# Performance work log

Hardware: AMD Instinct MI355X
Metric: run time of the kernel (lower is better)

The kernel has to match this reference:

```python
import jax, jax.numpy as jnp
import numpy as np

BETA = 0.25
EPS = 1e-12

def setup_inputs() -> dict:
    key = jax.random.key(0)
    k1, k2 = jax.random.split(key)
    f_BChw = jax.random.normal(k1, (32, 64, 32, 32), dtype=jnp.float32)
    emb_weight = jax.random.normal(k2, (8192, 64), dtype=jnp.float32)
    return {"f_BChw": f_BChw, "emb_weight": emb_weight}

def reference(f_BChw, emb_weight):
    f = f_BChw.astype(jnp.float32)
    B, C, h, w = f.shape
    V = emb_weight.shape[0]
    # flatten tokens: [B,C,h,w] -> [N,C]
    NxC = jnp.transpose(f, (0, 2, 3, 1)).reshape(-1, C)
    # cosine nearest-neighbor on detached, L2-normalized queries/codes
    q = jax.lax.stop_gradient(NxC)
    q = q / jnp.maximum(jnp.linalg.norm(q, axis=-1, keepdims=True), EPS)
    wn = emb_weight / jnp.maximum(jnp.linalg.norm(emb_weight, axis=-1, keepdims=True), EPS)
    sim = q @ wn.T                      # [N,V] -- dominant memory traffic
    idx_N = jnp.argmax(sim, axis=1)     # [N]
    # gather codes -> [B,C,h,w]
    fhat = emb_weight[idx_N].reshape(B, h, w, C).transpose(0, 3, 1, 2)
    sg = jax.lax.stop_gradient
    vq_loss = BETA * jnp.mean((sg(fhat) - f) ** 2) + jnp.mean((fhat - sg(f)) ** 2)
    # straight-through estimator
    fhat_out = f + sg(fhat - f)
    # usage statistics (bincount)
    counts = jnp.zeros((V,), jnp.float32).at[idx_N].add(1.0)
    prob = counts / counts.sum()
    vocab_usage = jnp.mean((prob > 0.01 / V).astype(jnp.float32)) * 100.0
    entropy_loss = jnp.float32(0.0)
    return fhat_out, vq_loss, entropy_loss, vocab_usage
```

## Files before the change

kernel.cpp:

```cpp
#include <hip/hip_runtime.h>

typedef _Float16 f16x8 __attribute__((ext_vector_type(8)));
typedef float f32x16 __attribute__((ext_vector_type(16)));

#define V_TOTAL 8192
#define C_DIM   64
#define N_TOK   32768
#define VSPLIT  4
#define VSEG    (V_TOTAL / VSPLIT)
#define CHUNKS  (VSEG / 32)
#define INV2048 4.8828125e-4f

typedef const __attribute__((address_space(1))) _Float16 glb_f16;
typedef __attribute__((address_space(3))) _Float16 lds_f16;


__device__ __forceinline__ unsigned long long packkey(float s, int idx) {
    unsigned u = __float_as_uint(s);
    unsigned k = u ^ ((unsigned)(((int)u) >> 31) | 0x80000000u);
    return ((unsigned long long)k << 32) | (unsigned)(8191 - idx);
}

__global__ __launch_bounds__(256)
void k_prep(const float* __restrict__ w, _Float16* __restrict__ cp,
            unsigned long long* __restrict__ keys, int* __restrict__ counts) {
    int v = blockIdx.x * 256 + threadIdx.x;
    counts[v] = 0;
#pragma unroll
    for (int i = 0; i < 4; ++i) keys[v * 4 + i] = 0ull;
    const float4* row = (const float4*)(w + v * C_DIM);
    float4 r[16];
    float s = 0.f;
#pragma unroll
    for (int i = 0; i < 16; ++i) {
        r[i] = row[i];
        s += r[i].x * r[i].x + r[i].y * r[i].y + r[i].z * r[i].z + r[i].w * r[i].w;
    }
    float inv = 1.0f / fmaxf(sqrtf(s), 1e-12f);
    const float* rs = (const float*)r;
    const int cv = v >> 5, c = v & 31;
#pragma unroll
    for (int q = 0; q < 8; ++q) {
        f16x8 hi, lo;
#pragma unroll
        for (int j = 0; j < 8; ++j) {
            float x = rs[q * 8 + j] * inv;
            _Float16 h = (_Float16)x;
            hi[j] = h;
            lo[j] = (_Float16)((x - (float)h) * 2048.0f);
        }
        *(f16x8*)(cp + cv * 4096 +        q * 256 + c * 8) = hi;
        *(f16x8*)(cp + cv * 4096 + 2048 + q * 256 + c * 8) = lo;
    }
}

__global__ __launch_bounds__(256, 4)
void k_argmax(const float* __restrict__ f, const _Float16* __restrict__ cp,
              unsigned long long* __restrict__ keys) {
    __shared__ __align__(16) _Float16 lds[2][4096];

    const int tid  = threadIdx.x;
    const int lane = tid & 63;
    const int wid  = tid >> 6;
    const int c31  = lane & 31;
    const int g    = lane >> 5;
    const int seg  = blockIdx.y;
    const int t0   = blockIdx.x * 128 + wid * 32;

    f16x8 bh[4], bl[4];
    {
        const int T = t0 + c31;
        const float* fb = f + (T >> 10) * 65536 + (T & 1023);
#pragma unroll
        for (int ks = 0; ks < 4; ++ks) {
#pragma unroll
            for (int j = 0; j < 8; ++j) {
                float v = fb[(ks * 16 + g * 8 + j) * 1024];
                _Float16 h = (_Float16)v;
                bh[ks][j] = h;
                bl[ks][j] = (_Float16)((v - (float)h) * 2048.0f);
            }
        }
    }

    const _Float16* seg_cp = cp + (size_t)seg * (CHUNKS * 4096);

    auto stage = [&](int cv, int buf) {
        const _Float16* src = seg_cp + cv * 4096 + wid * 1024 + lane * 8;
        _Float16* dst = &lds[buf][wid * 1024];
        __builtin_amdgcn_global_load_lds((glb_f16*)src,       (lds_f16*)dst,       16, 0, 0);
        __builtin_amdgcn_global_load_lds((glb_f16*)(src+512), (lds_f16*)(dst+512), 16, 0, 0);
    };

    f32x16 am = {0.f,0.f,0.f,0.f,0.f,0.f,0.f,0.f,0.f,0.f,0.f,0.f,0.f,0.f,0.f,0.f};
    f32x16 ac = am;

    float best = -3.4e38f;
    int   bidx = 0;

    stage(0, 0);
    __syncthreads();

    for (int cv = 0; cv < CHUNKS; ++cv) {
        if (cv + 1 < CHUNKS) stage(cv + 1, (cv + 1) & 1);

        const _Float16* base = &lds[cv & 1][g * 256 + c31 * 8];
#pragma unroll
        for (int ks = 0; ks < 4; ++ks) {
            f16x8 AH = *(const f16x8*)(base + ks * 512);
            f16x8 AL = *(const f16x8*)(base + 2048 + ks * 512);
            am = __builtin_amdgcn_mfma_f32_32x32x16_f16(AH, bh[ks], am, 0, 0, 0);
            ac = __builtin_amdgcn_mfma_f32_32x32x16_f16(AH, bl[ks], ac, 0, 0, 0);
            ac = __builtin_amdgcn_mfma_f32_32x32x16_f16(AL, bh[ks], ac, 0, 0, 0);
        }

        const int codebase = seg * VSEG + cv * 32;
#pragma unroll
        for (int r = 0; r < 16; ++r) {
            const int codeq = codebase + (r & 3) + 8 * (r >> 2);
            float s = fmaf(ac[r], INV2048, am[r]);
            bool u = s > best;
            best = u ? s : best;
            bidx = u ? codeq : bidx;
            am[r] = 0.f;
            ac[r] = 0.f;
        }
        __syncthreads();
    }

    bidx += 4 * g;
    {
        float ov = __shfl_xor(best, 32);
        int   oi = __shfl_xor(bidx, 32);
        if (ov > best || (ov == best && oi < bidx)) { best = ov; bidx = oi; }
    }
    if (lane < 32) {
        atomicMax(&keys[t0 + c31], packkey(best, bidx));
    }
}

__global__ __launch_bounds__(256)
void k_finalize(const float* __restrict__ f, const float* __restrict__ w,
                const unsigned long long* __restrict__ keys,
                int* __restrict__ counts, float* __restrict__ blocksq,
                float* __restrict__ out) {
    const int tid = threadIdx.x;
    const int t   = blockIdx.x * 256 + tid;

    const int bi = 8191 - (int)(unsigned)(keys[t] & 0xFFFFFFFFull);
    atomicAdd(&counts[bi], 1);

    float4 cr[16];
    const float4* crow = (const float4*)(w + bi * C_DIM);
#pragma unroll
    for (int i = 0; i < 16; ++i) cr[i] = crow[i];
    const float* crs = (const float*)cr;

    const int bb = t >> 10;
    const int hw = t & 1023;
    const float* fb = f + bb * 65536 + hw;
    float*       ob = out + bb * 65536 + hw;

    float s = 0.f;
#pragma unroll
    for (int c = 0; c < C_DIM; ++c) {
        float fv = fb[c * 1024];
        float fh = crs[c];
        float d  = fh - fv;
        s += d * d;
        ob[c * 1024] = fv + d;
    }

    __shared__ float red[256];
    red[tid] = s;
    __syncthreads();
    for (int st = 128; st > 0; st >>= 1) {
        if (tid < st) red[tid] += red[tid + st];
        __syncthreads();
    }
    if (tid == 0) blocksq[blockIdx.x] = red[0];
}

__global__ __launch_bounds__(256)
void k_stats(const int* __restrict__ counts, const float* __restrict__ blocksq,
             float* __restrict__ out) {
    __shared__ float redf[256];
    __shared__ int   redi[256];
    const int tid = threadIdx.x;
    int used = 0;
    for (int v = tid; v < V_TOTAL; v += 256) used += (counts[v] > 0) ? 1 : 0;
    redi[tid] = used;
    redf[tid] = (tid < 128) ? blocksq[tid] : 0.f;
    __syncthreads();
    for (int st = 128; st > 0; st >>= 1) {
        if (tid < st) { redi[tid] += redi[tid + st]; redf[tid] += redf[tid + st]; }
        __syncthreads();
    }
    if (tid == 0) {
        float mse = redf[0] / 2097152.0f;
        out[2097152] = 0.25f * mse + mse;
        out[2097153] = 0.0f;
        out[2097154] = 100.0f * (float)redi[0] / 8192.0f;
    }
}

extern "C" void kernel_launch(void* const* d_in, const int* in_sizes, int n_in,
                              void* d_out, int out_size, void* d_ws, size_t ws_size,
                              hipStream_t stream) {
    const float* f = (const float*)d_in[0];
    const float* w = (const float*)d_in[1];
    float* out = (float*)d_out;
    float* ws  = (float*)d_ws;

    _Float16*           cp      = (_Float16*)ws;
    unsigned long long* keys    = (unsigned long long*)(ws + 524288);
    int*                counts  = (int*)(ws + 589824);
    float*              blocksq = ws + 598016;

    hipLaunchKernelGGL(k_prep, dim3(32), dim3(256), 0, stream, w, cp, keys, counts);
    hipLaunchKernelGGL(k_argmax, dim3(N_TOK / 128, VSPLIT), dim3(256), 0, stream,
                       f, cp, keys);
    hipLaunchKernelGGL(k_finalize, dim3(128), dim3(256), 0, stream,
                       f, w, keys, counts, blocksq, out);
    hipLaunchKernelGGL(k_stats, dim3(1), dim3(256), 0, stream,
                       counts, blocksq, out);
}
```

Baseline: 123.4 us.

## Two-pass argmax: fp16 screening with top-2 margin, exact rescoring of ambiguous tokens

Replaces the single split-fp16 (hi+lo, three MFMAs per step) argmax with a cheap first pass. That pass uses only hi fp16 products, tracks the top two scores per token, and deepens LDS staging to four buffers with explicit vmcnt waits. A classify kernel merges the per-segment top-2 values and accepts a token when the margin exceeds a threshold scaled by the query norm. Otherwise it appends the token to a list that a second kernel rescans with the full hi/lo precision. This aims to cut the MFMA work by about a third for most tokens. The cost is two extra launches, extra workspace traffic, and correctness that depends on the error-bound threshold holding.

```diff
diff --git a/kernel.cpp b/kernel.cpp
--- a/kernel.cpp
+++ b/kernel.cpp
@@ -6,10 +6,15 @@
 #define V_TOTAL 8192
 #define C_DIM   64
 #define N_TOK   32768
-#define VSPLIT  4
-#define VSEG    (V_TOTAL / VSPLIT)
-#define CHUNKS  (VSEG / 32)
 #define INV2048 4.8828125e-4f
+#define THR_COEF 2.2e-3f
+
+#define VSPLIT1 4
+#define VSEG1   2048
+#define CH1     32
+#define VSPLIT2 8
+#define VSEG2   1024
+#define CH2     32
 
 typedef const __attribute__((address_space(1))) _Float16 glb_f16;
 typedef __attribute__((address_space(3))) _Float16 lds_f16;
@@ -23,9 +28,11 @@
 
 __global__ __launch_bounds__(256)
 void k_prep(const float* __restrict__ w, _Float16* __restrict__ cp,
-            unsigned long long* __restrict__ keys, int* __restrict__ counts) {
+            unsigned long long* __restrict__ keys, int* __restrict__ counts,
+            int* __restrict__ unc_cnt) {
     int v = blockIdx.x * 256 + threadIdx.x;
     counts[v] = 0;
+    if (v == 0) unc_cnt[0] = 0;
 #pragma unroll
     for (int i = 0; i < 4; ++i) keys[v * 4 + i] = 0ull;
     const float4* row = (const float4*)(w + v * C_DIM);
@@ -55,9 +62,10 @@
 }
 
 __global__ __launch_bounds__(256, 4)
-void k_argmax(const float* __restrict__ f, const _Float16* __restrict__ cp,
-              unsigned long long* __restrict__ keys) {
-    __shared__ __align__(16) _Float16 lds[2][4096];
+void k_pass1(const float* __restrict__ f, const _Float16* __restrict__ cp,
+             float* __restrict__ m1s, float* __restrict__ m2s,
+             int* __restrict__ i1s, float* __restrict__ fn2) {
+    __shared__ __align__(16) _Float16 lds[4][4096];
 
     const int tid  = threadIdx.x;
     const int lane = tid & 63;
@@ -67,7 +75,8 @@
     const int seg  = blockIdx.y;
     const int t0   = blockIdx.x * 128 + wid * 32;
 
-    f16x8 bh[4], bl[4];
+    f16x8 bh[4];
+    float s2 = 0.f;
     {
         const int T = t0 + c31;
         const float* fb = f + (T >> 10) * 65536 + (T & 1023);
@@ -76,78 +85,213 @@
 #pragma unroll
             for (int j = 0; j < 8; ++j) {
                 float v = fb[(ks * 16 + g * 8 + j) * 1024];
-                _Float16 h = (_Float16)v;
-                bh[ks][j] = h;
-                bl[ks][j] = (_Float16)((v - (float)h) * 2048.0f);
+                s2 += v * v;
+                bh[ks][j] = (_Float16)v;
             }
         }
     }
 
-    const _Float16* seg_cp = cp + (size_t)seg * (CHUNKS * 4096);
-
-    auto stage = [&](int cv, int buf) {
-        const _Float16* src = seg_cp + cv * 4096 + wid * 1024 + lane * 8;
-        _Float16* dst = &lds[buf][wid * 1024];
-        __builtin_amdgcn_global_load_lds((glb_f16*)src,       (lds_f16*)dst,       16, 0, 0);
-        __builtin_amdgcn_global_load_lds((glb_f16*)(src+512), (lds_f16*)(dst+512), 16, 0, 0);
+    const _Float16* seg_cp = cp + (size_t)seg * (VSEG1 / 32) * 4096;
+
+    auto stage = [&](int cv) {
+        const _Float16* s0 = seg_cp + (2 * cv + 0) * 4096 + wid * 512 + lane * 8;
+        const _Float16* s1 = seg_cp + (2 * cv + 1) * 4096 + wid * 512 + lane * 8;
+        _Float16* d0 = &lds[cv & 3][wid * 512];
+        _Float16* d1 = &lds[cv & 3][2048 + wid * 512];
+        __builtin_amdgcn_global_load_lds((glb_f16*)s0, (lds_f16*)d0, 16, 0, 0);
+        __builtin_amdgcn_global_load_lds((glb_f16*)s1, (lds_f16*)d1, 16, 0, 0);
     };
 
-    f32x16 am = {0.f,0.f,0.f,0.f,0.f,0.f,0.f,0.f,0.f,0.f,0.f,0.f,0.f,0.f,0.f,0.f};
-    f32x16 ac = am;
-
-    float best = -3.4e38f;
-    int   bidx = 0;
-
-    stage(0, 0);
-    __syncthreads();
-
-    for (int cv = 0; cv < CHUNKS; ++cv) {
-        if (cv + 1 < CHUNKS) stage(cv + 1, (cv + 1) & 1);
-
-        const _Float16* base = &lds[cv & 1][g * 256 + c31 * 8];
-#pragma unroll
-        for (int ks = 0; ks < 4; ++ks) {
-            f16x8 AH = *(const f16x8*)(base + ks * 512);
-            f16x8 AL = *(const f16x8*)(base + 2048 + ks * 512);
-            am = __builtin_amdgcn_mfma_f32_32x32x16_f16(AH, bh[ks], am, 0, 0, 0);
-            ac = __builtin_amdgcn_mfma_f32_32x32x16_f16(AH, bl[ks], ac, 0, 0, 0);
-            ac = __builtin_amdgcn_mfma_f32_32x32x16_f16(AL, bh[ks], ac, 0, 0, 0);
-        }
-
-        const int codebase = seg * VSEG + cv * 32;
-#pragma unroll
-        for (int r = 0; r < 16; ++r) {
-            const int codeq = codebase + (r & 3) + 8 * (r >> 2);
-            float s = fmaf(ac[r], INV2048, am[r]);
-            bool u = s > best;
-            best = u ? s : best;
-            bidx = u ? codeq : bidx;
-            am[r] = 0.f;
-            ac[r] = 0.f;
-        }
-        __syncthreads();
-    }
-
-    bidx += 4 * g;
+    const f32x16 zacc = {0.f,0.f,0.f,0.f,0.f,0.f,0.f,0.f,0.f,0.f,0.f,0.f,0.f,0.f,0.f,0.f};
+
+    float m1 = -3.4e38f, m2 = -3.4e38f;
+    int   i1 = 0;
+
+    stage(0); stage(1); stage(2);
+
+#pragma unroll 1
+    for (int cv = 0; cv < CH1; ++cv) {
+        if (cv < CH1 - 2)       asm volatile("s_waitcnt vmcnt(4)" ::: "memory");
+        else if (cv == CH1 - 2) asm volatile("s_waitcnt vmcnt(2)" ::: "memory");
+        else                    asm volatile("s_waitcnt vmcnt(0)" ::: "memory");
+        __builtin_amdgcn_s_barrier();
+        if (cv + 3 < CH1) stage(cv + 3);
+
+        const _Float16* base = &lds[cv & 3][g * 256 + c31 * 8];
+#pragma unroll
+        for (int tile = 0; tile < 2; ++tile) {
+            const _Float16* tb = base + tile * 2048;
+            f16x8 A0 = *(const f16x8*)(tb);
+            f16x8 A1 = *(const f16x8*)(tb + 512);
+            f16x8 A2 = *(const f16x8*)(tb + 1024);
+            f16x8 A3 = *(const f16x8*)(tb + 1536);
+            f32x16 amA, amB;
+            amA = __builtin_amdgcn_mfma_f32_32x32x16_f16(A0, bh[0], zacc, 0, 0, 0);
+            amB = __builtin_amdgcn_mfma_f32_32x32x16_f16(A2, bh[2], zacc, 0, 0, 0);
+            amA = __builtin_amdgcn_mfma_f32_32x32x16_f16(A1, bh[1], amA, 0, 0, 0);
+            amB = __builtin_amdgcn_mfma_f32_32x32x16_f16(A3, bh[3], amB, 0, 0, 0);
+
+            const int codebase = seg * VSEG1 + cv * 64 + tile * 32;
+#pragma unroll
+            for (int r = 0; r < 16; ++r) {
+                const int codeq = codebase + (r & 3) + 8 * (r >> 2);
+                float s = amA[r] + amB[r];
+                float nm2 = __builtin_amdgcn_fmed3f(m1, m2, s);
+                bool u = s > m1;
+                i1 = u ? codeq : i1;
+                m1 = fmaxf(m1, s);
+                m2 = nm2;
+            }
+        }
+    }
+
+    i1 += 4 * g;
     {
-        float ov = __shfl_xor(best, 32);
-        int   oi = __shfl_xor(bidx, 32);
-        if (ov > best || (ov == best && oi < bidx)) { best = ov; bidx = oi; }
+        float om1 = __shfl_xor(m1, 32);
+        float om2 = __shfl_xor(m2, 32);
+        int   oi1 = __shfl_xor(i1, 32);
+        float nm2 = fmaxf(fminf(m1, om1), fmaxf(m2, om2));
+        bool rep = om1 > m1;
+        i1 = rep ? oi1 : i1;
+        m1 = fmaxf(m1, om1);
+        m2 = nm2;
+        float os2 = __shfl_xor(s2, 32);
+        s2 += os2;
     }
     if (lane < 32) {
-        atomicMax(&keys[t0 + c31], packkey(best, bidx));
+        const int t = t0 + c31;
+        m1s[seg * N_TOK + t] = m1;
+        m2s[seg * N_TOK + t] = m2;
+        i1s[seg * N_TOK + t] = i1;
+        fn2[t] = s2;
+    }
+}
+
+__global__ __launch_bounds__(256)
+void k_classify(const float* __restrict__ m1s, const float* __restrict__ m2s,
+                const int* __restrict__ i1s, const float* __restrict__ fn2,
+                int* __restrict__ idxf, int* __restrict__ unc_list,
+                int* __restrict__ unc_cnt) {
+    const int t = blockIdx.x * 256 + threadIdx.x;
+    float a1 = m1s[t], a2 = m2s[t];
+    int   ai = i1s[t];
+#pragma unroll
+    for (int s = 1; s < VSPLIT1; ++s) {
+        float b1 = m1s[s * N_TOK + t];
+        float b2 = m2s[s * N_TOK + t];
+        int   bi = i1s[s * N_TOK + t];
+        float na2 = fmaxf(fminf(a1, b1), fmaxf(a2, b2));
+        bool rep = b1 > a1;
+        ai = rep ? bi : ai;
+        a1 = fmaxf(a1, b1);
+        a2 = na2;
+    }
+    const float thr = THR_COEF * sqrtf(fn2[t]);
+    if (a1 - a2 > thr) {
+        idxf[t] = ai;
+    } else {
+        idxf[t] = -1;
+        int pos = atomicAdd(unc_cnt, 1);
+        unc_list[pos] = t;
+    }
+}
+
+__global__ __launch_bounds__(64, 2)
+void k_pass2(const float* __restrict__ f, const _Float16* __restrict__ cp,
+             const int* __restrict__ unc_list, const int* __restrict__ unc_cnt,
+             unsigned long long* __restrict__ keys) {
+    const int lane = threadIdx.x;
+    const int c31  = lane & 31;
+    const int g    = lane >> 5;
+    const int seg  = blockIdx.y;
+
+    const int n = unc_cnt[0];
+    const int ngroups = (n + 31) >> 5;
+    const f32x16 zacc = {0.f,0.f,0.f,0.f,0.f,0.f,0.f,0.f,0.f,0.f,0.f,0.f,0.f,0.f,0.f,0.f};
+
+    for (int grp = blockIdx.x; grp < ngroups; grp += 256) {
+        int j = grp * 32 + c31;
+        if (j >= n) j = n - 1;
+        const int T = unc_list[j];
+
+        f16x8 bhh[4], bll[4];
+        {
+            const float* fb = f + (T >> 10) * 65536 + (T & 1023);
+#pragma unroll
+            for (int ks = 0; ks < 4; ++ks) {
+#pragma unroll
+                for (int jj = 0; jj < 8; ++jj) {
+                    float v = fb[(ks * 16 + g * 8 + jj) * 1024];
+                    _Float16 h = (_Float16)v;
+                    bhh[ks][jj] = h;
+                    bll[ks][jj] = (_Float16)((v - (float)h) * 2048.0f);
+                }
+            }
+        }
+
+        float best = -3.4e38f;
+        int   bidx = 0;
+
+#pragma unroll 1
+        for (int cv = 0; cv < CH2; ++cv) {
+            const _Float16* Ab = cp + (size_t)(seg * 32 + cv) * 4096 + g * 256 + c31 * 8;
+            f16x8 Ah0 = *(const f16x8*)(Ab);
+            f16x8 Ah1 = *(const f16x8*)(Ab + 512);
+            f16x8 Ah2 = *(const f16x8*)(Ab + 1024);
+            f16x8 Ah3 = *(const f16x8*)(Ab + 1536);
+            f16x8 Al0 = *(const f16x8*)(Ab + 2048);
+            f16x8 Al1 = *(const f16x8*)(Ab + 2560);
+            f16x8 Al2 = *(const f16x8*)(Ab + 3072);
+            f16x8 Al3 = *(const f16x8*)(Ab + 3584);
+
+            f32x16 amA, amB, acA, acB;
+            amA = __builtin_amdgcn_mfma_f32_32x32x16_f16(Ah0, bhh[0], zacc, 0, 0, 0);
+            amB = __builtin_amdgcn_mfma_f32_32x32x16_f16(Ah2, bhh[2], zacc, 0, 0, 0);
+            acA = __builtin_amdgcn_mfma_f32_32x32x16_f16(Ah0, bll[0], zacc, 0, 0, 0);
+            acB = __builtin_amdgcn_mfma_f32_32x32x16_f16(Ah2, bll[2], zacc, 0, 0, 0);
+            amA = __builtin_amdgcn_mfma_f32_32x32x16_f16(Ah1, bhh[1], amA, 0, 0, 0);
+            amB = __builtin_amdgcn_mfma_f32_32x32x16_f16(Ah3, bhh[3], amB, 0, 0, 0);
+            acA = __builtin_amdgcn_mfma_f32_32x32x16_f16(Al0, bhh[0], acA, 0, 0, 0);
+            acB = __builtin_amdgcn_mfma_f32_32x32x16_f16(Al2, bhh[2], acB, 0, 0, 0);
+            acA = __builtin_amdgcn_mfma_f32_32x32x16_f16(Ah1, bll[1], acA, 0, 0, 0);
+            acB = __builtin_amdgcn_mfma_f32_32x32x16_f16(Ah3, bll[3], acB, 0, 0, 0);
+            acA = __builtin_amdgcn_mfma_f32_32x32x16_f16(Al1, bhh[1], acA, 0, 0, 0);
+            acB = __builtin_amdgcn_mfma_f32_32x32x16_f16(Al3, bhh[3], acB, 0, 0, 0);
+
+            const int codebase = seg * VSEG2 + cv * 32;
+#pragma unroll
+            for (int r = 0; r < 16; ++r) {
+                const int codeq = codebase + (r & 3) + 8 * (r >> 2);
+                float s = fmaf(acA[r] + acB[r], INV2048, amA[r] + amB[r]);
+                bool u = s > best;
+                best = u ? s : best;
+                bidx = u ? codeq : bidx;
+            }
+        }
+
+        bidx += 4 * g;
+        {
+            float ov = __shfl_xor(best, 32);
+            int   oi = __shfl_xor(bidx, 32);
+            if (ov > best || (ov == best && oi < bidx)) { best = ov; bidx = oi; }
+        }
+        if (lane < 32) {
+            atomicMax(&keys[T], packkey(best, bidx));
+        }
     }
 }
 
 __global__ __launch_bounds__(256)
 void k_finalize(const float* __restrict__ f, const float* __restrict__ w,
                 const unsigned long long* __restrict__ keys,
+                const int* __restrict__ idxf,
                 int* __restrict__ counts, float* __restrict__ blocksq,
                 float* __restrict__ out) {
     const int tid = threadIdx.x;
     const int t   = blockIdx.x * 256 + tid;
 
-    const int bi = 8191 - (int)(unsigned)(keys[t] & 0xFFFFFFFFull);
+    int bi = idxf[t];
+    if (bi < 0) bi = 8191 - (int)(unsigned)(keys[t] & 0xFFFFFFFFull);
     atomicAdd(&counts[bi], 1);
 
     float4 cr[16];
@@ -165,8 +309,7 @@
 #pragma unroll
     for (int c = 0; c < C_DIM; ++c) {
         float fv = fb[c * 1024];
-        float fh = crs[c];
-        float d  = fh - fv;
+        float d  = crs[c] - fv;
         s += d * d;
         ob[c * 1024] = fv + d;
     }
@@ -212,16 +355,28 @@
     float* out = (float*)d_out;
     float* ws  = (float*)d_ws;
 
-    _Float16*           cp      = (_Float16*)ws;
-    unsigned long long* keys    = (unsigned long long*)(ws + 524288);
-    int*                counts  = (int*)(ws + 589824);
-    float*              blocksq = ws + 598016;
-
-    hipLaunchKernelGGL(k_prep, dim3(32), dim3(256), 0, stream, w, cp, keys, counts);
-    hipLaunchKernelGGL(k_argmax, dim3(N_TOK / 128, VSPLIT), dim3(256), 0, stream,
-                       f, cp, keys);
-    hipLaunchKernelGGL(k_finalize, dim3(128), dim3(256), 0, stream,
-                       f, w, keys, counts, blocksq, out);
+    _Float16*           cp       = (_Float16*)ws;
+    float*              m1s      = ws + 524288;
+    float*              m2s      = ws + 655360;
+    int*                i1s      = (int*)(ws + 786432);
+    float*              fn2      = ws + 917504;
+    unsigned long long* keys     = (unsigned long long*)(ws + 950272);
+    int*                idxf     = (int*)(ws + 1015808);
+    int*                unc_list = (int*)(ws + 1048576);
+    int*                unc_cnt  = (int*)(ws + 1081344);
+    int*                counts   = (int*)(ws + 1081408);
+    float*              blocksq  = ws + 1089600;
+
+    hipLaunchKernelGGL(k_prep, dim3(32), dim3(256), 0, stream,
+                       w, cp, keys, counts, unc_cnt);
+    hipLaunchKernelGGL(k_pass1, dim3(N_TOK / 128, VSPLIT1), dim3(256), 0, stream,
+                       f, cp, m1s, m2s, i1s, fn2);
+    hipLaunchKernelGGL(k_classify, dim3(N_TOK / 256), dim3(256), 0, stream,
+                       m1s, m2s, i1s, fn2, idxf, unc_list, unc_cnt);
+    hipLaunchKernelGGL(k_pass2, dim3(256, VSPLIT2), dim3(64), 0, stream,
+                       f, cp, unc_list, unc_cnt, keys);
+    hipLaunchKernelGGL(k_finalize, dim3(N_TOK / 256), dim3(256), 0, stream,
+                       f, w, keys, idxf, counts, blocksq, out);
     hipLaunchKernelGGL(k_stats, dim3(1), dim3(256), 0, stream,
                        counts, blocksq, out);
 }
```

Result: slower. 126.3 us (+2.3%).
